# Kernel optimization log

Measured on AMD Instinct MI355X. Metric: run time of the kernel, lower is better.

## Reference

```python
import jax, jax.numpy as jnp
import numpy as np

ALLOWED_SPANLEN = 7
NEG = -10000.0      # init value for logalpha, matching torch fill_(-10000.)
MASK_NEG = -1e9     # additive mask for out-of-window span starts


def setup_inputs() -> dict:
    key = jax.random.key(0)
    k1, k2 = jax.random.split(key)
    B, L, T = 16, 128, 11  # batch, sent_len, tagset_size (9 tags + START + STOP)
    scores = jax.random.normal(k1, (B, L, L, T, T), dtype=jnp.float32)
    # mask holds sentence lengths in [L//2, L] (used as gather index into logalpha)
    mask = jax.random.randint(k2, (B,), L // 2, L + 1, dtype=jnp.int32)
    return {"scores": scores, "mask": mask}


def reference(scores, mask):
    """Semi-CRF forward DP (get_logloss_denominator).

    scores: (B, L, L, T, T) -- scores[b, j, i, y_prev, y] is the score of a span
            [j, i] labeled y, with previous segment label y_prev.
    mask:   (B,) sentence lengths.
    """
    B, L, _, T, _ = scores.shape
    K = ALLOWED_SPANLEN
    start_id, stop_id = T - 1, T - 2

    alpha0 = jnp.full((B, L + 1, T), NEG, dtype=scores.dtype)
    alpha0 = alpha0.at[:, 0, start_id].set(0.0)

    # Re-index scores by span-end position so scan can stream one end per step.
    scores_by_end = jnp.moveaxis(scores, 2, 0)  # (L_end, B, L_start, T, T)
    offs = jnp.arange(K)

    def step(alpha, xs):
        i, sc = xs                # i in [1..L]; sc: (B, L, Tprev, Tcur), end = i-1
        js = i - K + offs         # candidate span starts: [i-K, i-1]
        valid = (js >= 0)[None, :, None, None]
        jsc = jnp.clip(js, 0, L - 1)
        a_w = jnp.take(alpha, jsc, axis=1)   # (B, K, Tprev)
        s_w = jnp.take(sc, jsc, axis=1)      # (B, K, Tprev, Tcur)
        t = jnp.where(valid, s_w + a_w[:, :, :, None], MASK_NEG)
        new = jax.nn.logsumexp(t, axis=(1, 2))           # (B, Tcur)
        alpha = jax.lax.dynamic_update_slice(alpha, new[:, None, :], (0, i, 0))
        return alpha, None

    alpha, _ = jax.lax.scan(step, alpha0, (jnp.arange(1, L + 1), scores_by_end))
    # gather logalpha at the sentence-length position for each batch element
    final = alpha[jnp.arange(B), mask, :]                # (B, T)
    return final[:, stop_id].sum()
```

## Files before the change

### kernel.cpp

```cpp
#include <hip/hip_runtime.h>
#include <math.h>

#define LL 128
#define TT 11
#define NP 121
#define KK 7
#define GS 20
#define SPW 240
#define NSLOT 8
#define PANEF 1024

#define LOG2E 1.4426950408889634f
#define LN2   0.6931471805599453f

__device__ __forceinline__ float fast_exp2(float x) { return __builtin_amdgcn_exp2f(x); }
__device__ __forceinline__ float fast_log2(float x) { return __builtin_amdgcn_logf(x); }
#if __has_builtin(__builtin_amdgcn_rcpf)
__device__ __forceinline__ float fast_rcp(float x) { return __builtin_amdgcn_rcpf(x); }
#else
__device__ __forceinline__ float fast_rcp(float x) { return 1.0f / x; }
#endif
__device__ __forceinline__ float rfl(float x) {
    return __int_as_float(__builtin_amdgcn_readfirstlane(__float_as_int(x)));
}
__device__ __forceinline__ void cfence() { __builtin_amdgcn_wave_barrier(); }
#define VMWAIT28() asm volatile("s_waitcnt vmcnt(28)" ::: "memory")
#define VMWAIT14() asm volatile("s_waitcnt vmcnt(14)" ::: "memory")
#define VMWAIT0()  asm volatile("s_waitcnt vmcnt(0)"  ::: "memory")
#define LGKM0()    asm volatile("s_waitcnt lgkmcnt(0)" ::: "memory")

__device__ __forceinline__ void block_sync() {
    asm volatile("" ::: "memory");
    __builtin_amdgcn_s_barrier();
    asm volatile("" ::: "memory");
}

__global__ __launch_bounds__(192, 1) void hscrf_pc2(const float* __restrict__ scores,
                                                    const int* __restrict__ mask,
                                                    float* __restrict__ out,
                                                    int n_batch)
{
    const int tid = threadIdx.x;
    const int l   = tid & 63;
    const int wid = tid >> 6;
    const int b   = blockIdx.x;
    if (b >= n_batch) return;

    __shared__ __align__(64) float ring[NSLOT][PANEF];
    __shared__ __align__(64) float sp[SPW];

    const float* sb = scores + (size_t)b * (size_t)(LL * (size_t)LL * NP);

    const int o1  = l + 64;
    const bool val1 = (o1 < NP);
    const int o1c = val1 ? o1 : 0;

    if (wid >= 1) {
        const int pw = wid - 1;

        float A0[KK], A1[KK], B0[KK], B1[KK], C0[KK], C1[KK];

        auto issue_pane = [&](int p, float (&a0)[KK], float (&a1)[KK]) {
#pragma unroll
            for (int k = 0; k < KK; ++k) {
                const int j = p - KK + k; const int jc = j < 0 ? 0 : j;
                const float* sl = sb + ((size_t)jc * LL + (size_t)(p - 1)) * NP;
                a0[k] = sl[l];
                a1[k] = sl[o1c];
            }
        };

        auto conv1 = [&](int p, const float (&a0)[KK], const float (&a1)[KK]) {
            const int slot = p & (NSLOT - 1);
            float v0[8], w1[8];
#pragma unroll
            for (int k = 0; k < KK; ++k) {
                const bool ok = (p - KK + k) >= 0;
                const float t0 = fast_exp2(a0[k] * LOG2E);
                const float t1 = fast_exp2(a1[k] * LOG2E);
                v0[k] = ok ? t0 : 0.0f;
                w1[k] = (ok && val1) ? t1 : 0.0f;
            }
            v0[7] = 0.0f; w1[7] = 0.0f;
            float4* dst = (float4*)&ring[slot][0];
            dst[l]       = make_float4(v0[0], v0[1], v0[2], v0[3]);
            dst[128 + l] = make_float4(v0[4], v0[5], v0[6], v0[7]);
            dst[64 + l]  = make_float4(w1[0], w1[1], w1[2], w1[3]);
            dst[192 + l] = make_float4(w1[4], w1[5], w1[6], w1[7]);
        };

        issue_pane(1 + pw, A0, A1);
        issue_pane(3 + pw, B0, B1);
        VMWAIT0();
        conv1(1 + pw, A0, A1);
        conv1(3 + pw, B0, B1);
        issue_pane(5 + pw, B0, B1);
        issue_pane(7 + pw, C0, C1);
        LGKM0(); block_sync();

        for (int t = 1; t <= 58; t += 3) {
            issue_pane(2 * t + 7 + pw, A0, A1);
            VMWAIT28();
            conv1(2 * t + 3 + pw, B0, B1);
            LGKM0(); block_sync();

            issue_pane(2 * t + 9 + pw, B0, B1);
            VMWAIT28();
            conv1(2 * t + 5 + pw, C0, C1);
            LGKM0(); block_sync();

            issue_pane(2 * t + 11 + pw, C0, C1);
            VMWAIT28();
            conv1(2 * t + 7 + pw, A0, A1);
            LGKM0(); block_sync();
        }
        VMWAIT14();
        conv1(125 + pw, B0, B1);
        LGKM0(); block_sync();
        VMWAIT0();
        conv1(127 + pw, C0, C1);
        LGKM0(); block_sync();
        block_sync();
        block_sync();
    } else {
        const int y0 = l % TT,   yp0 = l / TT;
        const int y1 = o1c % TT, yp1 = o1c / TT;
        const int i0w = y0 * GS + yp0;
        const int i1w = val1 ? (y1 * GS + yp1) : (220 + (l - 57));

        if (l < TT) sp[l * GS + 11] = 0.0f;

        const int mb = mask[b];

        float W0[KK], W1[KK];
#pragma unroll
        for (int k = 0; k < KK; ++k) { W0[k] = 0.0f; W1[k] = 0.0f; }
        W0[KK - 1] = (yp0 == TT - 1) ? 1.0f : 0.0f;
        W1[KK - 1] = (val1 && yp1 == TT - 1) ? 1.0f : 0.0f;

        float Cc = 0.0f;
        float saved = 0.0f;

        block_sync();

        const float4* ep1 = (const float4*)&ring[1][0];
        float4 ea0 = ep1[l],      ea1 = ep1[128 + l];
        float4 eb0 = ep1[64 + l], eb1 = ep1[192 + l];

        auto body = [&](int i) {
            float p0 = fmaf(ea0.x, W0[0], ea0.y * W0[1]);
            float q0 = fmaf(ea0.z, W0[2], ea0.w * W0[3]);
            float u0 = fmaf(ea1.x, W0[4], ea1.y * W0[5]);
            float s0 = (p0 + q0) + fmaf(ea1.z, W0[6], u0);
            float p1 = fmaf(eb0.x, W1[0], eb0.y * W1[1]);
            float q1 = fmaf(eb0.z, W1[2], eb0.w * W1[3]);
            float u1 = fmaf(eb1.x, W1[4], eb1.y * W1[5]);
            float s1 = (p1 + q1) + fmaf(eb1.z, W1[6], u1);
            sp[i0w] = s0;
            sp[i1w] = s1;

            cfence();

            const float4 qa0 = *(const float4*)(sp + yp0 * GS);
            const float4 qb0 = *(const float4*)(sp + yp0 * GS + 4);
            const float4 qc0 = *(const float4*)(sp + yp0 * GS + 8);
            const float4 qa1 = *(const float4*)(sp + yp1 * GS);
            const float4 qb1 = *(const float4*)(sp + yp1 * GS + 4);
            const float4 qc1 = *(const float4*)(sp + yp1 * GS + 8);

            const int ns = (i + 1) & (NSLOT - 1);
            const float4* ep = (const float4*)&ring[ns][0];
            const float4 na0 = ep[l],      na1 = ep[128 + l];
            const float4 nb0 = ep[64 + l], nb1 = ep[192 + l];

            const float SA = (((qa0.x + qa0.y) + (qa0.z + qa0.w)) +
                              ((qb0.x + qb0.y) + (qb0.z + qb0.w))) +
                             ((qc0.x + qc0.y) + (qc0.z + qc0.w));
            const float SB = (((qa1.x + qa1.y) + (qa1.z + qa1.w)) +
                              ((qb1.x + qb1.y) + (qb1.z + qb1.w))) +
                             ((qc1.x + qc1.y) + (qc1.z + qc1.w));

            const float s0u = rfl(SA);
            const float r = fast_rcp(s0u);

            saved = (i == mb) ? Cc + fast_log2(SB) : saved;
            Cc += fast_log2(s0u);

#pragma unroll
            for (int k = 0; k < KK - 1; ++k) { W0[k] = W0[k + 1] * r; W1[k] = W1[k + 1] * r; }
            W0[KK - 1] = SA * r;
            W1[KK - 1] = SB * r;

            ea0 = na0; ea1 = na1; eb0 = nb0; eb1 = nb1;

            cfence();
        };

        for (int i = 1; i <= LL; i += 2) {
            body(i);
            body(i + 1);
            block_sync();
        }

        if (l == 35) {
            atomicAdd(out, saved * LN2);
        }
    }
}

extern "C" void kernel_launch(void* const* d_in, const int* in_sizes, int n_in,
                              void* d_out, int out_size, void* d_ws, size_t ws_size,
                              hipStream_t stream) {
    const float* scores = (const float*)d_in[0];
    const int*   mask   = (const int*)d_in[1];
    float* out = (float*)d_out;
    const int B = in_sizes[1];

    hipMemsetAsync(out, 0, sizeof(float) * out_size, stream);

    (void)d_ws; (void)ws_size;

    hscrf_pc2<<<B, 192, 0, stream>>>(scores, mask, out, B);
}
```

Baseline: 185.1 us.

## Halve block barriers by converting two panes per producer step

Producer waves now load and convert two panes per stage with a two-buffer register rotation, so the consumer wave can process four DP steps between block barriers instead of two. The consumer prefetches ring slots in batches, raises its wave priority, and defers the log of the saved sum until the end. This cuts barrier count and moves the log off the per-step critical path. The cost is more live registers and tighter ring slot reuse, since four slots are now in flight per sync with eight slots total.

```diff
diff --git a/kernel.cpp b/kernel.cpp
--- a/kernel.cpp
+++ b/kernel.cpp
@@ -25,7 +25,6 @@
 }
 __device__ __forceinline__ void cfence() { __builtin_amdgcn_wave_barrier(); }
 #define VMWAIT28() asm volatile("s_waitcnt vmcnt(28)" ::: "memory")
-#define VMWAIT14() asm volatile("s_waitcnt vmcnt(14)" ::: "memory")
 #define VMWAIT0()  asm volatile("s_waitcnt vmcnt(0)"  ::: "memory")
 #define LGKM0()    asm volatile("s_waitcnt lgkmcnt(0)" ::: "memory")
 
@@ -35,7 +34,7 @@
     asm volatile("" ::: "memory");
 }
 
-__global__ __launch_bounds__(192, 1) void hscrf_pc2(const float* __restrict__ scores,
+__global__ __launch_bounds__(192, 1) void hscrf_pc3(const float* __restrict__ scores,
                                                     const int* __restrict__ mask,
                                                     float* __restrict__ out,
                                                     int n_batch)
@@ -58,7 +57,8 @@
     if (wid >= 1) {
         const int pw = wid - 1;
 
-        float A0[KK], A1[KK], B0[KK], B1[KK], C0[KK], C1[KK];
+        float Xa0[KK], Xa1[KK], Xb0[KK], Xb1[KK];
+        float Ya0[KK], Ya1[KK], Yb0[KK], Yb1[KK];
 
         auto issue_pane = [&](int p, float (&a0)[KK], float (&a1)[KK]) {
 #pragma unroll
@@ -68,6 +68,11 @@
                 a0[k] = sl[l];
                 a1[k] = sl[o1c];
             }
+        };
+        auto issue_pair = [&](int base, float (&a0)[KK], float (&a1)[KK],
+                              float (&b0)[KK], float (&b1)[KK]) {
+            issue_pane(base,     a0, a1);
+            issue_pane(base + 2, b0, b1);
         };
 
         auto conv1 = [&](int p, const float (&a0)[KK], const float (&a1)[KK]) {
@@ -88,40 +93,32 @@
             dst[64 + l]  = make_float4(w1[0], w1[1], w1[2], w1[3]);
             dst[192 + l] = make_float4(w1[4], w1[5], w1[6], w1[7]);
         };
-
-        issue_pane(1 + pw, A0, A1);
-        issue_pane(3 + pw, B0, B1);
+        auto conv_pair = [&](int base, const float (&a0)[KK], const float (&a1)[KK],
+                             const float (&b0)[KK], const float (&b1)[KK]) {
+            conv1(base,     a0, a1);
+            conv1(base + 2, b0, b1);
+        };
+
+        issue_pair(1 + pw, Xa0, Xa1, Xb0, Xb1);
         VMWAIT0();
-        conv1(1 + pw, A0, A1);
-        conv1(3 + pw, B0, B1);
-        issue_pane(5 + pw, B0, B1);
-        issue_pane(7 + pw, C0, C1);
+        conv_pair(1 + pw, Xa0, Xa1, Xb0, Xb1);
+        issue_pair(5 + pw, Xa0, Xa1, Xb0, Xb1);
         LGKM0(); block_sync();
 
-        for (int t = 1; t <= 58; t += 3) {
-            issue_pane(2 * t + 7 + pw, A0, A1);
+        for (int t = 1; t <= 29; t += 2) {
+            issue_pair(4 * t + 5 + pw, Ya0, Ya1, Yb0, Yb1);
             VMWAIT28();
-            conv1(2 * t + 3 + pw, B0, B1);
+            conv_pair(4 * t + 1 + pw, Xa0, Xa1, Xb0, Xb1);
             LGKM0(); block_sync();
 
-            issue_pane(2 * t + 9 + pw, B0, B1);
+            issue_pair(4 * t + 9 + pw, Xa0, Xa1, Xb0, Xb1);
             VMWAIT28();
-            conv1(2 * t + 5 + pw, C0, C1);
-            LGKM0(); block_sync();
-
-            issue_pane(2 * t + 11 + pw, C0, C1);
-            VMWAIT28();
-            conv1(2 * t + 7 + pw, A0, A1);
+            conv_pair(4 * t + 5 + pw, Ya0, Ya1, Yb0, Yb1);
             LGKM0(); block_sync();
         }
-        VMWAIT14();
-        conv1(125 + pw, B0, B1);
+        VMWAIT0();
+        conv_pair(125 + pw, Xa0, Xa1, Xb0, Xb1);
         LGKM0(); block_sync();
-        VMWAIT0();
-        conv1(127 + pw, C0, C1);
-        LGKM0(); block_sync();
-        block_sync();
-        block_sync();
     } else {
         const int y0 = l % TT,   yp0 = l / TT;
         const int y1 = o1c % TT, yp1 = o1c / TT;
@@ -139,15 +136,14 @@
         W1[KK - 1] = (val1 && yp1 == TT - 1) ? 1.0f : 0.0f;
 
         float Cc = 0.0f;
-        float saved = 0.0f;
-
+        float savedS = 1.0f;
+        float savedC = 0.0f;
+
+        __builtin_amdgcn_s_setprio(1);
         block_sync();
 
-        const float4* ep1 = (const float4*)&ring[1][0];
-        float4 ea0 = ep1[l],      ea1 = ep1[128 + l];
-        float4 eb0 = ep1[64 + l], eb1 = ep1[192 + l];
-
-        auto body = [&](int i) {
+        auto body = [&](int i, const float4& ea0, const float4& ea1,
+                               const float4& eb0, const float4& eb1) {
             float p0 = fmaf(ea0.x, W0[0], ea0.y * W0[1]);
             float q0 = fmaf(ea0.z, W0[2], ea0.w * W0[3]);
             float u0 = fmaf(ea1.x, W0[4], ea1.y * W0[5]);
@@ -168,11 +164,6 @@
             const float4 qb1 = *(const float4*)(sp + yp1 * GS + 4);
             const float4 qc1 = *(const float4*)(sp + yp1 * GS + 8);
 
-            const int ns = (i + 1) & (NSLOT - 1);
-            const float4* ep = (const float4*)&ring[ns][0];
-            const float4 na0 = ep[l],      na1 = ep[128 + l];
-            const float4 nb0 = ep[64 + l], nb1 = ep[192 + l];
-
             const float SA = (((qa0.x + qa0.y) + (qa0.z + qa0.w)) +
                               ((qb0.x + qb0.y) + (qb0.z + qb0.w))) +
                              ((qc0.x + qc0.y) + (qc0.z + qc0.w));
@@ -183,7 +174,8 @@
             const float s0u = rfl(SA);
             const float r = fast_rcp(s0u);
 
-            saved = (i == mb) ? Cc + fast_log2(SB) : saved;
+            savedS = (i == mb) ? SB : savedS;
+            savedC = (i == mb) ? Cc : savedC;
             Cc += fast_log2(s0u);
 
 #pragma unroll
@@ -191,19 +183,37 @@
             W0[KK - 1] = SA * r;
             W1[KK - 1] = SB * r;
 
-            ea0 = na0; ea1 = na1; eb0 = nb0; eb1 = nb1;
-
             cfence();
         };
 
-        for (int i = 1; i <= LL; i += 2) {
-            body(i);
-            body(i + 1);
-            block_sync();
+        for (int t = 1; t <= 32; ++t) {
+            const int p0 = 4 * t - 3;
+
+            const float4* r0 = (const float4*)&ring[p0 & (NSLOT - 1)][0];
+            const float4* r1 = (const float4*)&ring[(p0 + 1) & (NSLOT - 1)][0];
+            const float4 Aa0 = r0[l], Aa1 = r0[128 + l];
+            const float4 Ab0 = r0[64 + l], Ab1 = r0[192 + l];
+            const float4 Ba0 = r1[l], Ba1 = r1[128 + l];
+            const float4 Bb0 = r1[64 + l], Bb1 = r1[192 + l];
+
+            body(p0, Aa0, Aa1, Ab0, Ab1);
+
+            const float4* r2 = (const float4*)&ring[(p0 + 2) & (NSLOT - 1)][0];
+            const float4* r3 = (const float4*)&ring[(p0 + 3) & (NSLOT - 1)][0];
+            const float4 Ca0 = r2[l], Ca1 = r2[128 + l];
+            const float4 Cb0 = r2[64 + l], Cb1 = r2[192 + l];
+            const float4 Da0 = r3[l], Da1 = r3[128 + l];
+            const float4 Db0 = r3[64 + l], Db1 = r3[192 + l];
+
+            body(p0 + 1, Ba0, Ba1, Bb0, Bb1);
+            body(p0 + 2, Ca0, Ca1, Cb0, Cb1);
+            body(p0 + 3, Da0, Da1, Db0, Db1);
+
+            if (t < 32) block_sync();
         }
 
         if (l == 35) {
-            atomicAdd(out, saved * LN2);
+            atomicAdd(out, (savedC + fast_log2(savedS)) * LN2);
         }
     }
 }
@@ -220,5 +230,5 @@
 
     (void)d_ws; (void)ws_size;
 
-    hscrf_pc2<<<B, 192, 0, stream>>>(scores, mask, out, B);
-}
+    hscrf_pc3<<<B, 192, 0, stream>>>(scores, mask, out, B);
+}
```

Result: faster. 177.6 us (-4.1%).
